# Kernel tuning notes

Hardware: AMD Instinct MI355X
Metric: run time of the kernel (lower is better)

## Reference

```python
import jax, jax.numpy as jnp
import numpy as np

N = 50000      # nodes
E = 800000     # edges (no self loops; reference appends one self loop per node implicitly)
D = 128        # input_dim
NUM_MSGS = 21
OUT = 63


def setup_inputs() -> dict:
    key = jax.random.key(0)
    ks = jax.random.split(key, 12)
    x = jax.random.normal(ks[0], (N, 1, D), dtype=jnp.float32)
    # edge_index with src != dst (remove_self_loops is then a no-op, faithful to torch module)
    src = jax.random.randint(ks[1], (E,), 0, N)
    off = jax.random.randint(ks[2], (E,), 1, N)
    dst = (src + off) % N
    edge_index = jnp.stack([src, dst]).astype(jnp.int64)
    batch = jnp.zeros((N,), dtype=jnp.int64)  # unused by forward
    s = 0.05
    W_msg = jax.random.normal(ks[3], (NUM_MSGS, D, D), dtype=jnp.float32) * s
    b_msg = jax.random.normal(ks[4], (NUM_MSGS, D), dtype=jnp.float32) * s
    W_upd = jax.random.normal(ks[5], (NUM_MSGS, D, 2 * D), dtype=jnp.float32) * s
    W1 = jax.random.normal(ks[6], (256, D), dtype=jnp.float32) * s
    b1 = jax.random.normal(ks[7], (256,), dtype=jnp.float32) * s
    W2 = jax.random.normal(ks[8], (128, 256), dtype=jnp.float32) * s
    b2 = jax.random.normal(ks[9], (128,), dtype=jnp.float32) * s
    W3 = jax.random.normal(ks[10], (OUT, 128), dtype=jnp.float32) * s
    b3 = jax.random.normal(ks[11], (OUT,), dtype=jnp.float32) * s
    return {"x": x, "edge_index": edge_index, "batch": batch,
            "W_msg": W_msg, "b_msg": b_msg, "W_upd": W_upd,
            "W1": W1, "b1": b1, "W2": W2, "b2": b2, "W3": W3, "b3": b3}


def reference(x, edge_index, batch, W_msg, b_msg, W_upd, W1, b1, W2, b2, W3, b3):
    x = x[:, 0, :]  # squeeze(1) -> [N, D]
    src, dst = edge_index[0], edge_index[1]

    def layer(h, p):
        Wm, bm, Wu = p
        # message is per-source-node: transform once per node, then gather
        m = jnp.tanh(h @ Wm.T + bm)                              # [N, D]
        # aggr='add' over edges + one self loop per node (add_self_loops)
        aggr = jax.ops.segment_sum(m[src], dst, num_segments=N) + m
        z = jnp.concatenate([aggr, h], axis=-1) @ Wu.T           # [N, D]
        return jax.nn.relu(z), None  # update ReLU; outer ReLU is idempotent

    h, _ = jax.lax.scan(layer, x, (W_msg, b_msg, W_upd))
    h = jax.nn.relu(h @ W1.T + b1)
    h = jax.nn.relu(h @ W2.T + b2)
    return h @ W3.T + b3  # [N, 63]
```

## Files before the change

### kernel.cpp

```cpp
#include <hip/hip_runtime.h>
#include <cstdint>

#define NN 50000
#define NE 800000

typedef __attribute__((ext_vector_type(8))) short    s16x8;
typedef __attribute__((ext_vector_type(4))) float    f32x4;
typedef __attribute__((ext_vector_type(4))) unsigned short u16x4;
typedef _Float16 f16x8 __attribute__((ext_vector_type(8)));

typedef unsigned short ushort_t;
typedef unsigned int   uint_t;

__device__ __forceinline__ unsigned short f2h(float v){
    _Float16 f = (_Float16)v; unsigned short u; __builtin_memcpy(&u, &f, 2); return u;
}
__device__ __forceinline__ float h2f(unsigned short u){
    _Float16 f; __builtin_memcpy(&f, &u, 2); return (float)f;
}

__global__ void hist_kernel(const int* __restrict__ dst, int* counts){
    int e = blockIdx.x * blockDim.x + threadIdx.x;
    if (e < NE) atomicAdd(&counts[dst[e]], 1);
}

__global__ void blocksum_kernel(const int* __restrict__ counts, int* __restrict__ bsum){
    __shared__ int sd[256];
    int i = blockIdx.x * 256 + threadIdx.x;
    int c = (i < NN) ? counts[i] : 0;
    sd[threadIdx.x] = c; __syncthreads();
    for (int o = 128; o > 0; o >>= 1){
        if (threadIdx.x < o) sd[threadIdx.x] += sd[threadIdx.x + o];
        __syncthreads();
    }
    if (threadIdx.x == 0) bsum[blockIdx.x] = sd[0];
}

__global__ void scanb_kernel(const int* __restrict__ bsum, int* __restrict__ boff,
                             int* __restrict__ row_start, int nb){
    __shared__ int sd[256];
    int t = threadIdx.x;
    int v = (t < nb) ? bsum[t] : 0;
    sd[t] = v; __syncthreads();
    for (int o = 1; o < 256; o <<= 1){
        int u = (t >= o) ? sd[t - o] : 0;
        __syncthreads();
        sd[t] += u;
        __syncthreads();
    }
    if (t < nb) boff[t] = sd[t] - v;
    if (t == 0) row_start[NN] = NE;
}

__global__ void localscan_kernel(const int* __restrict__ counts, const int* __restrict__ boff,
                                 int* __restrict__ row_start, int* __restrict__ cursor){
    __shared__ int sd[256];
    int t = threadIdx.x, i = blockIdx.x * 256 + t;
    int c = (i < NN) ? counts[i] : 0;
    sd[t] = c; __syncthreads();
    for (int o = 1; o < 256; o <<= 1){
        int u = (t >= o) ? sd[t - o] : 0;
        __syncthreads();
        sd[t] += u;
        __syncthreads();
    }
    if (i < NN){
        int ex = boff[blockIdx.x] + sd[t] - c;
        row_start[i] = ex; cursor[i] = ex;
    }
}

__global__ void scatter_kernel(const int* __restrict__ src, const int* __restrict__ dst,
                               int* cursor, int* __restrict__ colv){
    int e = blockIdx.x * blockDim.x + threadIdx.x;
    if (e < NE){
        int pos = atomicAdd(&cursor[dst[e]], 1);
        colv[pos] = src[e];
    }
}

__global__ void convert_x_kernel(const float* __restrict__ x, ushort_t* __restrict__ xf){
    int i = blockIdx.x * blockDim.x + threadIdx.x;
    if (i >= NN * 32) return;
    f32x4 v = *reinterpret_cast<const f32x4*>(x + (size_t)i * 4);
    u16x4 h;
#pragma unroll
    for (int j = 0; j < 4; ++j) h[j] = f2h(v[j]);
    *reinterpret_cast<u16x4*>(xf + (size_t)i * 4) = h;
}

__global__ void prep_wmsg(const float* __restrict__ W, ushort_t* __restrict__ hi,
                          ushort_t* __restrict__ lo){
    int idx = blockIdx.x * blockDim.x + threadIdx.x;
    const int per = 4 * 8 * 512;
    if (idx >= 21 * per) return;
    int layer = idx / per, r = idx % per;
    int kk = r / 4096, nt = (r / 512) & 7, lane = (r / 8) & 63, i = r & 7;
    int c = nt * 16 + (lane & 15);
    int k = kk * 32 + (lane >> 4) * 8 + i;
    float w = W[(size_t)layer * 16384 + c * 128 + k];
    unsigned short h = f2h(w);
    hi[idx] = h; lo[idx] = f2h(w - h2f(h));
}

__global__ void prep_wupd(const float* __restrict__ W, ushort_t* __restrict__ hi,
                          ushort_t* __restrict__ lo){
    int idx = blockIdx.x * blockDim.x + threadIdx.x;
    const int per = 8 * 8 * 512;
    if (idx >= 21 * per) return;
    int layer = idx / per, r = idx % per;
    int kk = r / 4096, nt = (r / 512) & 7, lane = (r / 8) & 63, i = r & 7;
    int c = nt * 16 + (lane & 15);
    int k = kk * 32 + (lane >> 4) * 8 + i;
    float w = W[(size_t)layer * 32768 + c * 256 + k];
    unsigned short h = f2h(w);
    hi[idx] = h; lo[idx] = f2h(w - h2f(h));
}

__global__ void prep_mlp(const float* __restrict__ W1, const float* __restrict__ W2,
                         const float* __restrict__ W3,
                         ushort_t* w1h, ushort_t* w1l,
                         ushort_t* w2h, ushort_t* w2l,
                         ushort_t* w3h, ushort_t* w3l){
    int idx = blockIdx.x * blockDim.x + threadIdx.x;
    if (idx >= 73728) return;
    const float* W; ushort_t *ph, *pl; int NT, Kld, nc, local;
    if (idx < 32768)      { local = idx;         W = W1; ph = w1h; pl = w1l; NT = 16; Kld = 128; nc = 256; }
    else if (idx < 65536) { local = idx - 32768; W = W2; ph = w2h; pl = w2l; NT = 8;  Kld = 256; nc = 128; }
    else                  { local = idx - 65536; W = W3; ph = w3h; pl = w3l; NT = 4;  Kld = 128; nc = 63;  }
    int i = local & 7, lane = (local >> 3) & 63, nt = (local >> 9) % NT, kk = local / (512 * NT);
    int c = nt * 16 + (lane & 15);
    int k = kk * 32 + (lane >> 4) * 8 + i;
    float w = (c < nc) ? W[c * Kld + k] : 0.f;
    unsigned short h = f2h(w);
    ph[local] = h; pl[local] = f2h(w - h2f(h));
}

template<int KK1, int KK2, int NT>
__device__ __forceinline__ void core_f16(
    const ushort_t* __restrict__ A1, const ushort_t* __restrict__ A2,
    const ushort_t* __restrict__ Bh, const ushort_t* __restrict__ Bl,
    int NTtot, int nt0, int waveRow0, int lane, f32x4 (&acc)[NT])
{
    const int lm = lane & 15;
    const int lk = (lane >> 4) * 8;
#pragma unroll
    for (int kk = 0; kk < KK1 + KK2; ++kk){
        const ushort_t* ap; int ld, kc;
        if (kk < KK1){ ap = A1; ld = KK1 * 32; kc = kk * 32 + lk; }
        else         { ap = A2; ld = KK2 * 32; kc = (kk - KK1) * 32 + lk; }
        f16x8 af = *reinterpret_cast<const f16x8*>(ap + (size_t)(waveRow0 + lm) * ld + kc);
        const ushort_t* bp = Bh + ((size_t)(kk * NTtot + nt0)) * 512 + lane * 8;
        const ushort_t* bq = Bl + ((size_t)(kk * NTtot + nt0)) * 512 + lane * 8;
#pragma unroll
        for (int nt = 0; nt < NT; ++nt){
            f16x8 bh = *reinterpret_cast<const f16x8*>(bp + nt * 512);
            f16x8 bl = *reinterpret_cast<const f16x8*>(bq + nt * 512);
            acc[nt] = __builtin_amdgcn_mfma_f32_16x16x32_f16(af, bh, acc[nt], 0, 0, 0);
            acc[nt] = __builtin_amdgcn_mfma_f32_16x16x32_f16(af, bl, acc[nt], 0, 0, 0);
        }
    }
}

#define LDS_STRIDE 136

template<int NT, int ACT, bool HAS_BIAS>
__device__ __forceinline__ void epi_stage(
    f32x4 (&acc)[NT], const float* __restrict__ bias, int colOffE,
    ushort_t* lds, int w, int lane)
{
    const int lm = lane & 15;
    const int cr = (lane >> 4) * 4;
#pragma unroll
    for (int nt = 0; nt < NT; ++nt){
        float bv = HAS_BIAS ? bias[colOffE + nt * 16 + lm] : 0.f;
#pragma unroll
        for (int j = 0; j < 4; ++j){
            float v = acc[nt][j] + bv;
            if (ACT == 1) v = v > 0.f ? v : 0.f;
            else if (ACT == 2) v = tanhf(v);
            lds[(w * 16 + cr + j) * LDS_STRIDE + nt * 16 + lm] = f2h(v);
        }
    }
}

__device__ __forceinline__ void flush_tile(
    const ushort_t* lds, ushort_t* __restrict__ out,
    int blockRow0, int ldcE, int colOffE, int tid)
{
#pragma unroll
    for (int it = 0; it < 4; ++it){
        int idx  = it * 256 + tid;
        int row  = idx >> 4;
        int colE = (idx & 15) * 8;
        int g = blockRow0 + row;
        if (g < NN)
            *reinterpret_cast<s16x8*>(out + (size_t)g * ldcE + colOffE + colE) =
                *reinterpret_cast<const s16x8*>(lds + row * LDS_STRIDE + colE);
    }
}

template<int KK1, int NT, int ACT, bool HAS_BIAS, int OUTMODE>
__global__ __launch_bounds__(256) void gemm_f16(
    const ushort_t* __restrict__ A1,
    const ushort_t* __restrict__ Bh, const ushort_t* __restrict__ Bl, int NTtot,
    const float* __restrict__ bias,
    ushort_t* __restrict__ Cs, float* __restrict__ Cf, int ldcE, int ncols)
{
    __shared__ ushort_t lds[64 * LDS_STRIDE];
    const int lane = threadIdx.x & 63;
    const int w    = threadIdx.x >> 6;
    const int nt0  = blockIdx.y * NT;
    const int colOffE = blockIdx.y * (NT * 16);
    const int waveRow0 = blockIdx.x * 64 + w * 16;
    f32x4 acc[NT];
#pragma unroll
    for (int nt = 0; nt < NT; ++nt)
#pragma unroll
        for (int j = 0; j < 4; ++j) acc[nt][j] = 0.f;
    core_f16<KK1, 0, NT>(A1, nullptr, Bh, Bl, NTtot, nt0, waveRow0, lane, acc);

    if constexpr (OUTMODE == 2){
        epi_stage<NT, ACT, HAS_BIAS>(acc, bias, colOffE, lds, w, lane);
        __syncthreads();
        flush_tile(lds, Cs, blockIdx.x * 64, ldcE, colOffE, threadIdx.x);
    } else {
        const int lm = lane & 15;
        const int cr = (lane >> 4) * 4;
#pragma unroll
        for (int nt = 0; nt < NT; ++nt){
            int col = colOffE + nt * 16 + lm;
            if (col >= ncols) continue;
            float bv = HAS_BIAS ? bias[col] : 0.f;
#pragma unroll
            for (int j = 0; j < 4; ++j){
                int g = waveRow0 + cr + j;
                if (g < NN){
                    float v = acc[nt][j] + bv;
                    if (ACT == 1) v = v > 0.f ? v : 0.f;
                    else if (ACT == 2) v = tanhf(v);
                    Cf[(size_t)g * ldcE + col] = v;
                }
            }
        }
    }
}

template<bool WITH_MSG>
__global__ __launch_bounds__(256) void fused_update_msg(
    const ushort_t* __restrict__ ag, const ushort_t* __restrict__ h,
    const ushort_t* __restrict__ Wuh, const ushort_t* __restrict__ Wul,
    const ushort_t* __restrict__ Wmh, const ushort_t* __restrict__ Wml,
    const float* __restrict__ bm,
    ushort_t* __restrict__ h_out, ushort_t* __restrict__ m_out)
{
    __shared__ ushort_t lds[64 * LDS_STRIDE];
    const int lane = threadIdx.x & 63;
    const int w    = threadIdx.x >> 6;
    const int waveRow0 = blockIdx.x * 64 + w * 16;
    const int lm = lane & 15;
    const int lk = (lane >> 4) * 8;

    f32x4 acc[8];
#pragma unroll
    for (int nt = 0; nt < 8; ++nt)
#pragma unroll
        for (int j = 0; j < 4; ++j) acc[nt][j] = 0.f;
    core_f16<4, 4, 8>(ag, h, Wuh, Wul, 8, 0, waveRow0, lane, acc);
    epi_stage<8, 1, false>(acc, nullptr, 0, lds, w, lane);
    __syncthreads();
    flush_tile(lds, h_out, blockIdx.x * 64, 128, 0, threadIdx.x);

    if constexpr (WITH_MSG){
        f32x4 acc2[8];
#pragma unroll
        for (int nt = 0; nt < 8; ++nt)
#pragma unroll
            for (int j = 0; j < 4; ++j) acc2[nt][j] = 0.f;
#pragma unroll
        for (int kk = 0; kk < 4; ++kk){
            f16x8 af = *reinterpret_cast<const f16x8*>(&lds[(w * 16 + lm) * LDS_STRIDE + kk * 32 + lk]);
            const ushort_t* bp = Wmh + (size_t)(kk * 8) * 512 + lane * 8;
            const ushort_t* bq = Wml + (size_t)(kk * 8) * 512 + lane * 8;
#pragma unroll
            for (int nt = 0; nt < 8; ++nt){
                f16x8 bh = *reinterpret_cast<const f16x8*>(bp + nt * 512);
                f16x8 bl = *reinterpret_cast<const f16x8*>(bq + nt * 512);
                acc2[nt] = __builtin_amdgcn_mfma_f32_16x16x32_f16(af, bh, acc2[nt], 0, 0, 0);
                acc2[nt] = __builtin_amdgcn_mfma_f32_16x16x32_f16(af, bl, acc2[nt], 0, 0, 0);
            }
        }
        __syncthreads();
        epi_stage<8, 2, true>(acc2, bm, 0, lds, w, lane);
        __syncthreads();
        flush_tile(lds, m_out, blockIdx.x * 64, 128, 0, threadIdx.x);
    }
}

__global__ __launch_bounds__(256) void aggregate_kernel(
    const ushort_t* __restrict__ m,
    const int* __restrict__ row_start, const int* __restrict__ cols,
    ushort_t* __restrict__ ag)
{
    int wid  = (blockIdx.x * 256 + threadIdx.x) >> 6;
    int lane = threadIdx.x & 63;
    int g    = lane >> 4;
    int fl   = lane & 15;
    int s0 = row_start[wid], s1 = row_start[wid + 1];

    float a[8];
#pragma unroll
    for (int j = 0; j < 8; ++j) a[j] = 0.f;

    if (g == 0){
        f16x8 v = *reinterpret_cast<const f16x8*>(m + (size_t)wid * 128 + fl * 8);
#pragma unroll
        for (int j = 0; j < 8; ++j) a[j] += (float)v[j];
    }

    int e = s0;
    for (; e + 15 < s1; e += 16){
        f16x8 v0 = *reinterpret_cast<const f16x8*>(m + (size_t)cols[e      + g] * 128 + fl * 8);
        f16x8 v1 = *reinterpret_cast<const f16x8*>(m + (size_t)cols[e + 4  + g] * 128 + fl * 8);
        f16x8 v2 = *reinterpret_cast<const f16x8*>(m + (size_t)cols[e + 8  + g] * 128 + fl * 8);
        f16x8 v3 = *reinterpret_cast<const f16x8*>(m + (size_t)cols[e + 12 + g] * 128 + fl * 8);
#pragma unroll
        for (int j = 0; j < 8; ++j)
            a[j] += ((float)v0[j] + (float)v1[j]) + ((float)v2[j] + (float)v3[j]);
    }
    for (; e + 7 < s1; e += 8){
        f16x8 v0 = *reinterpret_cast<const f16x8*>(m + (size_t)cols[e     + g] * 128 + fl * 8);
        f16x8 v1 = *reinterpret_cast<const f16x8*>(m + (size_t)cols[e + 4 + g] * 128 + fl * 8);
#pragma unroll
        for (int j = 0; j < 8; ++j) a[j] += (float)v0[j] + (float)v1[j];
    }
    for (; e < s1; e += 4){
        int idx = e + g;
        if (idx < s1){
            f16x8 v0 = *reinterpret_cast<const f16x8*>(m + (size_t)cols[idx] * 128 + fl * 8);
#pragma unroll
            for (int j = 0; j < 8; ++j) a[j] += (float)v0[j];
        }
    }

#pragma unroll
    for (int j = 0; j < 8; ++j){
        a[j] += __shfl_xor(a[j], 16);
        a[j] += __shfl_xor(a[j], 32);
    }

    if (g == 0){
        s16x8 outv;
#pragma unroll
        for (int j = 0; j < 8; ++j) outv[j] = (short)f2h(a[j]);
        *reinterpret_cast<s16x8*>(ag + (size_t)wid * 128 + fl * 8) = outv;
    }
}

extern "C" void kernel_launch(void* const* d_in, const int* in_sizes, int n_in,
                              void* d_out, int out_size, void* d_ws, size_t ws_size,
                              hipStream_t stream)
{
    const float* x     = (const float*)d_in[0];
    const int*   ei    = (const int*)d_in[1];
    const float* W_msg = (const float*)d_in[3];
    const float* b_msg = (const float*)d_in[4];
    const float* W_upd = (const float*)d_in[5];
    const float* W1    = (const float*)d_in[6];
    const float* b1    = (const float*)d_in[7];
    const float* W2    = (const float*)d_in[8];
    const float* b2    = (const float*)d_in[9];
    const float* W3    = (const float*)d_in[10];
    const float* b3    = (const float*)d_in[11];
    const int* srcp = ei;
    const int* dstp = ei + NE;

    char* ws = (char*)d_ws;
    size_t off = 0;
    auto carve = [&](size_t bytes) -> void* {
        void* p = ws + off;
        off += (bytes + 255) & ~(size_t)255;
        return p;
    };
    const size_t FBUF = (size_t)NN * 128 * 2;
    ushort_t* xf = (ushort_t*)carve(FBUF);
    ushort_t* hA = (ushort_t*)carve(FBUF);
    ushort_t* m  = (ushort_t*)carve(FBUF);
    ushort_t* ag = (ushort_t*)carve(FBUF);

    int* counts    = (int*)carve((size_t)NN * 4);
    int* cursor    = (int*)carve((size_t)NN * 4);
    int* row_start = (int*)carve(((size_t)NN + 1) * 4);
    int* bsum      = (int*)carve(256 * 4);
    int* boff      = (int*)carve(256 * 4);
    int* colv      = (int*)carve((size_t)NE * 4);

    ushort_t* wmsg_hi = (ushort_t*)carve((size_t)21 * 16384 * 2);
    ushort_t* wmsg_lo = (ushort_t*)carve((size_t)21 * 16384 * 2);
    ushort_t* wupd_hi = (ushort_t*)carve((size_t)21 * 32768 * 2);
    ushort_t* wupd_lo = (ushort_t*)carve((size_t)21 * 32768 * 2);
    ushort_t* w1_hi   = (ushort_t*)carve(32768 * 2);
    ushort_t* w1_lo   = (ushort_t*)carve(32768 * 2);
    ushort_t* w2_hi   = (ushort_t*)carve(32768 * 2);
    ushort_t* w2_lo   = (ushort_t*)carve(32768 * 2);
    ushort_t* w3_hi   = (ushort_t*)carve(8192 * 2);
    ushort_t* w3_lo   = (ushort_t*)carve(8192 * 2);
    (void)carve(65536);

    const int NB = (NN + 255) / 256;
    const int GB = (NN + 63) / 64;

    hipMemsetAsync(counts, 0, (size_t)NN * 4, stream);
    hist_kernel<<<(NE + 255) / 256, 256, 0, stream>>>(dstp, counts);
    blocksum_kernel<<<NB, 256, 0, stream>>>(counts, bsum);
    scanb_kernel<<<1, 256, 0, stream>>>(bsum, boff, row_start, NB);
    localscan_kernel<<<NB, 256, 0, stream>>>(counts, boff, row_start, cursor);
    scatter_kernel<<<(NE + 255) / 256, 256, 0, stream>>>(srcp, dstp, cursor, colv);

    convert_x_kernel<<<(NN * 32 + 255) / 256, 256, 0, stream>>>(x, xf);
    prep_wmsg<<<(21 * 16384 + 255) / 256, 256, 0, stream>>>(W_msg, wmsg_hi, wmsg_lo);
    prep_wupd<<<(21 * 32768 + 255) / 256, 256, 0, stream>>>(W_upd, wupd_hi, wupd_lo);
    prep_mlp<<<288, 256, 0, stream>>>(W1, W2, W3, w1_hi, w1_lo, w2_hi, w2_lo, w3_hi, w3_lo);

    gemm_f16<4, 8, 2, true, 2><<<GB, 256, 0, stream>>>(
        xf, wmsg_hi, wmsg_lo, 8, b_msg, m, nullptr, 128, 128);

    const ushort_t* cur = xf;
    ushort_t* nxt = hA;
    for (int l = 0; l < 21; ++l){
        aggregate_kernel<<<NN / 4, 256, 0, stream>>>(m, row_start, colv, ag);
        if (l < 20){
            fused_update_msg<true><<<GB, 256, 0, stream>>>(
                ag, cur,
                wupd_hi + (size_t)l * 32768, wupd_lo + (size_t)l * 32768,
                wmsg_hi + (size_t)(l + 1) * 16384, wmsg_lo + (size_t)(l + 1) * 16384,
                b_msg + (size_t)(l + 1) * 128,
                nxt, m);
        } else {
            fused_update_msg<false><<<GB, 256, 0, stream>>>(
                ag, cur,
                wupd_hi + (size_t)l * 32768, wupd_lo + (size_t)l * 32768,
                nullptr, nullptr, nullptr,
                nxt, nullptr);
        }
        const ushort_t* t = cur; cur = nxt; nxt = (ushort_t*)t;
    }

    ushort_t* h1 = m;
    gemm_f16<4, 8, 1, true, 2><<<dim3(GB, 2), 256, 0, stream>>>(
        cur, w1_hi, w1_lo, 16, b1, h1, nullptr, 256, 256);
    gemm_f16<8, 8, 1, true, 2><<<GB, 256, 0, stream>>>(
        h1, w2_hi, w2_lo, 8, b2, xf, nullptr, 128, 128);
    gemm_f16<4, 4, 0, true, 0><<<GB, 256, 0, stream>>>(
        xf, w3_hi, w3_lo, 4, b3, nullptr, (float*)d_out, 63, 63);
}
```

Before: 1.509 ms.

## Register-block fused update/message kernel over two 16-row tiles per wave

The fused update+message kernel now covers 128 rows per block, with each wave computing two 16-row M tiles. Every loaded weight fragment (hi and lo halves) feeds MFMAs for both tiles, which halves weight-fragment loads per output row in both the update and message GEMMs. The LDS staging buffer and the flush loop are doubled to 128 rows. In exchange the kernel holds twice as many accumulator registers and launches about half as many blocks, which can lower occupancy and leave CUs idle on a grid of roughly 391 blocks.

Result: slower. 1.673 ms (+10.9%).

```diff
diff --git a/kernel.cpp b/kernel.cpp
--- a/kernel.cpp
+++ b/kernel.cpp
@@ -167,7 +167,7 @@
 template<int NT, int ACT, bool HAS_BIAS>
 __device__ __forceinline__ void epi_stage(
     f32x4 (&acc)[NT], const float* __restrict__ bias, int colOffE,
-    ushort_t* lds, int w, int lane)
+    ushort_t* lds, int rowBase, int lane)
 {
     const int lm = lane & 15;
     const int cr = (lane >> 4) * 4;
@@ -179,17 +179,18 @@
             float v = acc[nt][j] + bv;
             if (ACT == 1) v = v > 0.f ? v : 0.f;
             else if (ACT == 2) v = tanhf(v);
-            lds[(w * 16 + cr + j) * LDS_STRIDE + nt * 16 + lm] = f2h(v);
-        }
-    }
-}
-
+            lds[(rowBase + cr + j) * LDS_STRIDE + nt * 16 + lm] = f2h(v);
+        }
+    }
+}
+
+template<int ROWS>
 __device__ __forceinline__ void flush_tile(
     const ushort_t* lds, ushort_t* __restrict__ out,
     int blockRow0, int ldcE, int colOffE, int tid)
 {
 #pragma unroll
-    for (int it = 0; it < 4; ++it){
+    for (int it = 0; it < ROWS / 16; ++it){
         int idx  = it * 256 + tid;
         int row  = idx >> 4;
         int colE = (idx & 15) * 8;
@@ -221,9 +222,9 @@
     core_f16<KK1, 0, NT>(A1, nullptr, Bh, Bl, NTtot, nt0, waveRow0, lane, acc);
 
     if constexpr (OUTMODE == 2){
-        epi_stage<NT, ACT, HAS_BIAS>(acc, bias, colOffE, lds, w, lane);
-        __syncthreads();
-        flush_tile(lds, Cs, blockIdx.x * 64, ldcE, colOffE, threadIdx.x);
+        epi_stage<NT, ACT, HAS_BIAS>(acc, bias, colOffE, lds, w * 16, lane);
+        __syncthreads();
+        flush_tile<64>(lds, Cs, blockIdx.x * 64, ldcE, colOffE, threadIdx.x);
     } else {
         const int lm = lane & 15;
         const int cr = (lane >> 4) * 4;
@@ -254,46 +255,74 @@
     const float* __restrict__ bm,
     ushort_t* __restrict__ h_out, ushort_t* __restrict__ m_out)
 {
-    __shared__ ushort_t lds[64 * LDS_STRIDE];
+    __shared__ ushort_t lds[128 * LDS_STRIDE];
     const int lane = threadIdx.x & 63;
     const int w    = threadIdx.x >> 6;
-    const int waveRow0 = blockIdx.x * 64 + w * 16;
+    const int blockRow0 = blockIdx.x * 128;
+    const int waveRow0  = blockRow0 + w * 32;
     const int lm = lane & 15;
     const int lk = (lane >> 4) * 8;
 
-    f32x4 acc[8];
-#pragma unroll
-    for (int nt = 0; nt < 8; ++nt)
-#pragma unroll
-        for (int j = 0; j < 4; ++j) acc[nt][j] = 0.f;
-    core_f16<4, 4, 8>(ag, h, Wuh, Wul, 8, 0, waveRow0, lane, acc);
-    epi_stage<8, 1, false>(acc, nullptr, 0, lds, w, lane);
+    f32x4 acc[2][8];
+#pragma unroll
+    for (int mi = 0; mi < 2; ++mi)
+#pragma unroll
+        for (int nt = 0; nt < 8; ++nt)
+#pragma unroll
+            for (int j = 0; j < 4; ++j) acc[mi][nt][j] = 0.f;
+
+#pragma unroll
+    for (int kk = 0; kk < 8; ++kk){
+        const ushort_t* ap = (kk < 4) ? ag : h;
+        int kc = (kk < 4) ? kk * 32 + lk : (kk - 4) * 32 + lk;
+        f16x8 af0 = *reinterpret_cast<const f16x8*>(ap + (size_t)(waveRow0 + lm) * 128 + kc);
+        f16x8 af1 = *reinterpret_cast<const f16x8*>(ap + (size_t)(waveRow0 + 16 + lm) * 128 + kc);
+        const ushort_t* bp = Wuh + (size_t)(kk * 8) * 512 + lane * 8;
+        const ushort_t* bq = Wul + (size_t)(kk * 8) * 512 + lane * 8;
+#pragma unroll
+        for (int nt = 0; nt < 8; ++nt){
+            f16x8 bh = *reinterpret_cast<const f16x8*>(bp + nt * 512);
+            f16x8 bl = *reinterpret_cast<const f16x8*>(bq + nt * 512);
+            acc[0][nt] = __builtin_amdgcn_mfma_f32_16x16x32_f16(af0, bh, acc[0][nt], 0, 0, 0);
+            acc[0][nt] = __builtin_amdgcn_mfma_f32_16x16x32_f16(af0, bl, acc[0][nt], 0, 0, 0);
+            acc[1][nt] = __builtin_amdgcn_mfma_f32_16x16x32_f16(af1, bh, acc[1][nt], 0, 0, 0);
+            acc[1][nt] = __builtin_amdgcn_mfma_f32_16x16x32_f16(af1, bl, acc[1][nt], 0, 0, 0);
+        }
+    }
+    epi_stage<8, 1, false>(acc[0], nullptr, 0, lds, w * 32,      lane);
+    epi_stage<8, 1, false>(acc[1], nullptr, 0, lds, w * 32 + 16, lane);
     __syncthreads();
-    flush_tile(lds, h_out, blockIdx.x * 64, 128, 0, threadIdx.x);
+    flush_tile<128>(lds, h_out, blockRow0, 128, 0, threadIdx.x);
 
     if constexpr (WITH_MSG){
-        f32x4 acc2[8];
-#pragma unroll
-        for (int nt = 0; nt < 8; ++nt)
-#pragma unroll
-            for (int j = 0; j < 4; ++j) acc2[nt][j] = 0.f;
+        f32x4 acc2[2][8];
+#pragma unroll
+        for (int mi = 0; mi < 2; ++mi)
+#pragma unroll
+            for (int nt = 0; nt < 8; ++nt)
+#pragma unroll
+                for (int j = 0; j < 4; ++j) acc2[mi][nt][j] = 0.f;
 #pragma unroll
         for (int kk = 0; kk < 4; ++kk){
-            f16x8 af = *reinterpret_cast<const f16x8*>(&lds[(w * 16 + lm) * LDS_STRIDE + kk * 32 + lk]);
+            f16x8 af0 = *reinterpret_cast<const f16x8*>(&lds[(w * 32 + lm)      * LDS_STRIDE + kk * 32 + lk]);
+            f16x8 af1 = *reinterpret_cast<const f16x8*>(&lds[(w * 32 + 16 + lm) * LDS_STRIDE + kk * 32 + lk]);
             const ushort_t* bp = Wmh + (size_t)(kk * 8) * 512 + lane * 8;
             const ushort_t* bq = Wml + (size_t)(kk * 8) * 512 + lane * 8;
 #pragma unroll
             for (int nt = 0; nt < 8; ++nt){
                 f16x8 bh = *reinterpret_cast<const f16x8*>(bp + nt * 512);
                 f16x8 bl = *reinterpret_cast<const f16x8*>(bq + nt * 512);
-                acc2[nt] = __builtin_amdgcn_mfma_f32_16x16x32_f16(af, bh, acc2[nt], 0, 0, 0);
-                acc2[nt] = __builtin_amdgcn_mfma_f32_16x16x32_f16(af, bl, acc2[nt], 0, 0, 0);
+                acc2[0][nt] = __builtin_amdgcn_mfma_f32_16x16x32_f16(af0, bh, acc2[0][nt], 0, 0, 0);
+                acc2[0][nt] = __builtin_amdgcn_mfma_f32_16x16x32_f16(af0, bl, acc2[0][nt], 0, 0, 0);
+                acc2[1][nt] = __builtin_amdgcn_mfma_f32_16x16x32_f16(af1, bh, acc2[1][nt], 0, 0, 0);
+                acc2[1][nt] = __builtin_amdgcn_mfma_f32_16x16x32_f16(af1, bl, acc2[1][nt], 0, 0, 0);
             }
         }
         __syncthreads();
-        epi_stage<8, 2, true>(acc2, bm, 0, lds, w, lane);
-        __syncthreads();
-        flush_tile(lds, m_out, blockIdx.x * 64, 128, 0, threadIdx.x);
+        epi_stage<8, 2, true>(acc2[0], bm, 0, lds, w * 32,      lane);
+        epi_stage<8, 2, true>(acc2[1], bm, 0, lds, w * 32 + 16, lane);
+        __syncthreads();
+        flush_tile<128>(lds, m_out, blockRow0, 128, 0, threadIdx.x);
     }
 }
 
@@ -407,8 +436,9 @@
     ushort_t* w3_lo   = (ushort_t*)carve(8192 * 2);
     (void)carve(65536);
 
-    const int NB = (NN + 255) / 256;
-    const int GB = (NN + 63) / 64;
+    const int NB  = (NN + 255) / 256;
+    const int GB  = (NN + 63) / 64;
+    const int GBF = (NN + 127) / 128;
 
     hipMemsetAsync(counts, 0, (size_t)NN * 4, stream);
     hist_kernel<<<(NE + 255) / 256, 256, 0, stream>>>(dstp, counts);
@@ -430,14 +460,14 @@
     for (int l = 0; l < 21; ++l){
         aggregate_kernel<<<NN / 4, 256, 0, stream>>>(m, row_start, colv, ag);
         if (l < 20){
-            fused_update_msg<true><<<GB, 256, 0, stream>>>(
+            fused_update_msg<true><<<GBF, 256, 0, stream>>>(
                 ag, cur,
                 wupd_hi + (size_t)l * 32768, wupd_lo + (size_t)l * 32768,
                 wmsg_hi + (size_t)(l + 1) * 16384, wmsg_lo + (size_t)(l + 1) * 16384,
                 b_msg + (size_t)(l + 1) * 128,
                 nxt, m);
         } else {
-            fused_update_msg<false><<<GB, 256, 0, stream>>>(
+            fused_update_msg<false><<<GBF, 256, 0, stream>>>(
                 ag, cur,
                 wupd_hi + (size_t)l * 32768, wupd_lo + (size_t)l * 32768,
                 nullptr, nullptr, nullptr,
```
